# Performance work log

Measured on AMD Instinct MI355X. Metric: run time of the kernel, lower is better.

The kernel has to match this reference:

```python
import jax, jax.numpy as jnp
import numpy as np

# Log-barrier hyperparameters (match torch module defaults / init_kwargs)
K_ITER = 30
MU = 0.01
LR = 1.0
BACKTRACK = 0.5
MAX_LS = 25
EPS = 1e-06

B, S, M, N = 32, 16, 128, 256


def setup_inputs() -> dict:
    key = jax.random.key(0)
    k1, k2, k3 = jax.random.split(key, 3)
    A = jax.random.uniform(k1, (B, S, M, N), dtype=jnp.float32)  # nonnegative rows
    x_star = jax.random.uniform(k2, (B, S, N), dtype=jnp.float32)  # interior point
    b = jnp.einsum('bsmn,bsn->bsm', A, x_star) + 0.5  # strictly feasible polytope
    x_raw = jax.random.normal(k3, (B, S, N), dtype=jnp.float32)
    lower = jnp.zeros((B, S, N), dtype=jnp.float32)
    return {"x_raw": x_raw, "A": A, "b": b, "lower": lower}


def _feasible(x, A_w, b_w, lower):
    # strict feasibility: A x <= b - eps and x >= lower + eps   -> [B,S,1] bool
    Ax = jnp.einsum('bsmn,bsn->bsm', A_w, x)
    c1 = jnp.all(Ax <= b_w - EPS, axis=-1, keepdims=True)
    c2 = jnp.all(x >= lower + EPS, axis=-1, keepdims=True)
    return c1 & c2


def reference(x_raw, A, b, lower):
    # row-normalize constraints (row_normalize=True)
    row_norm = jnp.maximum(jnp.linalg.norm(A, axis=-1, keepdims=True), 1e-12)
    A_w = A / row_norm
    b_w = b / row_norm[..., 0]

    # Deterministic interior-point init (replaces per-sample CPU cvxpy Chebyshev LP):
    # x = lower + t*1 with t = 0.5 * max step along ones-direction staying feasible.
    Ad = jnp.sum(A_w, axis=-1)                                   # [B,S,m] = A_w @ 1
    s = b_w - jnp.einsum('bsmn,bsn->bsm', A_w, lower)            # slack at lower
    ratio = jnp.where(Ad > 0, s / jnp.maximum(Ad, 1e-12), jnp.inf)
    t = 0.5 * jnp.min(ratio, axis=-1, keepdims=True)             # [B,S,1]
    t = jnp.maximum(t, 2.0 * EPS)
    x = lower + t

    # feasibility repair branch (faithful to module; no-op for our inputs)
    feas = _feasible(x, A_w, b_w, lower)
    x = jnp.where(feas, x, 0.5 * (jnp.maximum(x, 0.0) + lower))

    steps = LR * (BACKTRACK ** jnp.arange(MAX_LS, dtype=jnp.float32))  # [L]

    def body(x, _):
        Ax = jnp.einsum('bsmn,bsn->bsm', A_w, x)
        slack = jnp.maximum(b_w - Ax, 1e-12)
        g_bar = jnp.einsum('bsmn,bsm->bsn', A_w, MU / slack)
        s_lo = jnp.maximum(x - lower, 1e-12)
        grad = (x - x_raw) + g_bar + MU / s_lo

        # backtracking line search with GLOBAL ok.all() acceptance (as in torch)
        cand = x[None] - steps[:, None, None, None] * grad[None]       # [L,B,S,n]
        Axc = jnp.einsum('bsmn,lbsn->lbsm', A_w, cand)
        ok = (jnp.all(Axc <= b_w[None] - EPS, axis=-1)
              & jnp.all(cand >= (lower + EPS)[None], axis=-1))          # [L,B,S]
        ok_all = jnp.all(ok, axis=(1, 2))                               # [L]
        found = jnp.any(ok_all)
        idx = jnp.argmax(ok_all)                                        # first accepted step
        w = jax.nn.one_hot(idx, MAX_LS, dtype=x.dtype) * found.astype(x.dtype)
        x_new = jnp.tensordot(w, cand, axes=1) + (1.0 - found.astype(x.dtype)) * x
        return x_new, None

    x, _ = jax.lax.scan(body, x, None, length=K_ITER)
    return jnp.maximum(x, 0.0)
```

## Files before the change

kernel.cpp:

```cpp
#include <hip/hip_runtime.h>

#define K_ITER   30
#define MU       0.01f
#define EPS      1e-6f
#define MAX_LS   25
#define FULLMASK 0x01FFFFFFu
#define MM       128
#define NN       256
#define NPROB    512
#define NTHR     512

#define LSTRIDE 32
#define NBC     16
#define W_FLAG(p)  ((p)*LSTRIDE)
#define W_BCAST(i) (NPROB*LSTRIDE + (i)*LSTRIDE)
#define W_END      (NPROB*LSTRIDE + NBC*LSTRIDE)

#define RED64_AND(v) do { v &= __shfl_xor(v, 1);  v &= __shfl_xor(v, 2);  v &= __shfl_xor(v, 4); \
                          v &= __shfl_xor(v, 8);  v &= __shfl_xor(v, 16); v &= __shfl_xor(v, 32); } while (0)
#define RED64_OR(v)  do { v |= __shfl_xor(v, 1);  v |= __shfl_xor(v, 2);  v |= __shfl_xor(v, 4); \
                          v |= __shfl_xor(v, 8);  v |= __shfl_xor(v, 16); v |= __shfl_xor(v, 32); } while (0)
#define RED64_MIN(v) do { v = fminf(v, __shfl_xor(v, 1));  v = fminf(v, __shfl_xor(v, 2)); \
                          v = fminf(v, __shfl_xor(v, 4));  v = fminf(v, __shfl_xor(v, 8)); \
                          v = fminf(v, __shfl_xor(v, 16)); v = fminf(v, __shfl_xor(v, 32)); } while (0)

#define AGLOAD(p)     __hip_atomic_load((p),      __ATOMIC_RELAXED, __HIP_MEMORY_SCOPE_AGENT)
#define AGSTORE(p, v) __hip_atomic_store((p), (v), __ATOMIC_RELAXED, __HIP_MEMORY_SCOPE_AGENT)

__device__ __forceinline__ float red16_add(float v) {
    v += __int_as_float(__builtin_amdgcn_update_dpp(0, __float_as_int(v), 0x128, 0xF, 0xF, false));
    v += __int_as_float(__builtin_amdgcn_update_dpp(0, __float_as_int(v), 0x124, 0xF, 0xF, false));
    v += __int_as_float(__builtin_amdgcn_update_dpp(0, __float_as_int(v), 0x122, 0xF, 0xF, false));
    v += __int_as_float(__builtin_amdgcn_update_dpp(0, __float_as_int(v), 0x121, 0xF, 0xF, false));
    return v;
}

__global__ void lbp_ws_init(unsigned* __restrict__ wsu)
{
    const int idx = blockIdx.x * 1024 + threadIdx.x;
    if (idx < W_END) wsu[idx] = 0u;
}

__global__ __launch_bounds__(NTHR, 4)
void lbp_fused(const float* __restrict__ xraw_g,
               const float* __restrict__ A_g,
               const float* __restrict__ b_g,
               const float* __restrict__ lower_g,
               float* __restrict__ out_g,
               unsigned* __restrict__ wsu)
{
    const int p    = blockIdx.x;
    const int t    = threadIdx.x;
    const int lane = t & 63;
    const int wave = t >> 6;
    const int g    = lane >> 4;
    const int j    = lane & 15;
    const int wb   = wave * 16;

    const float* A = A_g + (size_t)p * (MM * NN);

    __shared__ __align__(16) float s_x[NN];
    __shared__ __align__(16) float s_grad[NN];
    __shared__ __align__(16) float s_xraw[NN];
    __shared__ __align__(16) float s_lower[NN];
    __shared__ __align__(16) float s_p1g[32][NN];
    __shared__ float s_pg[MM], s_px[MM];
    __shared__ float s_redw[8];
    __shared__ unsigned s_redu[8];
    __shared__ unsigned s_mask, s_gm;
    __shared__ float s_step, s_t0;

    float4 a[4][4];
    {
        const float* base = A + (size_t)(wb + 4 * g) * NN + 4 * j;
        #pragma unroll
        for (int r = 0; r < 4; ++r)
            #pragma unroll
            for (int c = 0; c < 4; ++c)
                a[r][c] = *(const float4*)(base + r * NN + 64 * c);
    }

    if (t < NN) { s_xraw[t] = xraw_g[p * NN + t]; s_lower[t] = lower_g[p * NN + t]; }

    float bbr[4];
    #pragma unroll
    for (int r = 0; r < 4; ++r) bbr[r] = b_g[p * MM + wb + 4 * g + r];

    const float stepj0 = ldexpf(1.0f, -j);

    if (t == 0) { s_mask = 0xFFFFFFFFu; s_step = 0.0f; }
    __syncthreads();

    float cer[4], clr[4];
    {
        float ssq[4] = {0.f,0.f,0.f,0.f}, rs[4] = {0.f,0.f,0.f,0.f}, al[4] = {0.f,0.f,0.f,0.f};
        #pragma unroll
        for (int c = 0; c < 4; ++c) {
            const float4 lo4 = ((const float4*)s_lower)[j + 16 * c];
            #pragma unroll
            for (int r = 0; r < 4; ++r) {
                const float4 av = a[r][c];
                ssq[r] += av.x*av.x + av.y*av.y + av.z*av.z + av.w*av.w;
                rs[r]  += av.x + av.y + av.z + av.w;
                al[r]  += av.x*lo4.x + av.y*lo4.y + av.z*lo4.z + av.w*lo4.w;
            }
        }
        float alr[4], rsr[4];
        float rmin = INFINITY;
        #pragma unroll
        for (int r = 0; r < 4; ++r) {
            const float ssqs = red16_add(ssq[r]);
            const float rss  = red16_add(rs[r]);
            const float als  = red16_add(al[r]);
            const float rr = fmaxf(sqrtf(ssqs), 1e-12f);
            clr[r] = 1e-12f * rr;
            cer[r] = bbr[r] - EPS * rr;
            const float adw = rss / rr;
            const float sw  = (bbr[r] - als) / rr;
            const float ratio = (adw > 0.f) ? (sw / fmaxf(adw, 1e-12f)) : INFINITY;
            rmin = fminf(rmin, ratio);
            alr[r] = als; rsr[r] = rss;
        }
        RED64_MIN(rmin);
        if (lane == 0) s_redw[wave] = rmin;
        __syncthreads();
        if (t == 0) {
            float m = s_redw[0];
            #pragma unroll
            for (int w = 1; w < 8; ++w) m = fminf(m, s_redw[w]);
            s_t0 = fmaxf(0.5f * m, 2.0f * EPS);
        }
        __syncthreads();
        const float t0v = s_t0;
        float xi = 0.f;
        if (t < NN) { xi = s_lower[t] + t0v; s_x[t] = xi; }
        float axc0[4];
        #pragma unroll
        for (int r = 0; r < 4; ++r) {
            axc0[r] = alr[r] + t0v * rsr[r];
            if (j == 0) { s_px[wb + 4 * g + r] = axc0[r]; s_pg[wb + 4 * g + r] = 0.f; }
        }

        int okf = 1;
        #pragma unroll
        for (int r = 0; r < 4; ++r) okf = okf && (axc0[r] <= cer[r]);
        if (t < NN) okf = okf && (xi >= s_lower[t] + EPS);
        const int feas = __syncthreads_and(okf);
        if (!feas) {
            if (t < NN) s_x[t] = 0.5f * (fmaxf(s_x[t], 0.f) + s_lower[t]);
            __syncthreads();
            float axp[4] = {0.f,0.f,0.f,0.f};
            #pragma unroll
            for (int c = 0; c < 4; ++c) {
                const float4 x4 = ((const float4*)s_x)[j + 16 * c];
                #pragma unroll
                for (int r = 0; r < 4; ++r) {
                    const float4 av = a[r][c];
                    axp[r] += av.x*x4.x + av.y*x4.y + av.z*x4.z + av.w*x4.w;
                }
            }
            #pragma unroll
            for (int r = 0; r < 4; ++r) {
                const float s = red16_add(axp[r]);
                if (j == 0) s_px[wb + 4 * g + r] = s;
            }
            __syncthreads();
        }
    }

    for (int k = 0; k < K_ITER; ++k) {
        {
            const float stp = s_step;
            float wm[4];
            #pragma unroll
            for (int r = 0; r < 4; ++r) {
                const int m = wb + 4 * g + r;
                const float axm = s_px[m] - stp * s_pg[m];
                wm[r] = MU / fmaxf(bbr[r] - axm, clr[r]);
            }
            #pragma unroll
            for (int c = 0; c < 4; ++c) {
                float4 gb;
                gb.x = a[0][c].x*wm[0] + a[1][c].x*wm[1] + a[2][c].x*wm[2] + a[3][c].x*wm[3];
                gb.y = a[0][c].y*wm[0] + a[1][c].y*wm[1] + a[2][c].y*wm[2] + a[3][c].y*wm[3];
                gb.z = a[0][c].z*wm[0] + a[1][c].z*wm[1] + a[2][c].z*wm[2] + a[3][c].z*wm[3];
                gb.w = a[0][c].w*wm[0] + a[1][c].w*wm[1] + a[2][c].w*wm[2] + a[3][c].w*wm[3];
                ((float4*)s_p1g[wave * 4 + g])[j + 16 * c] = gb;
            }
        }
        __syncthreads();

        if (t < NN) {
            float gsum = 0.f;
            #pragma unroll
            for (int q = 0; q < 32; ++q) gsum += s_p1g[q][t];
            const float xt = s_x[t];
            const float gr = (xt - s_xraw[t]) + gsum + MU / fmaxf(xt - s_lower[t], 1e-12f);
            s_grad[t] = gr;
            unsigned mn = 0u;
            const float loe = s_lower[t] + EPS;
            float st = 1.0f;
            #pragma unroll
            for (int l = 0; l < MAX_LS; ++l) {
                if (xt - st * gr >= loe) mn |= (1u << l);
                st *= 0.5f;
            }
            RED64_AND(mn);
            if (lane == 0) atomicAnd(&s_mask, mn);
        }
        __syncthreads();

        {
            float pg[4] = {0.f,0.f,0.f,0.f}, px[4] = {0.f,0.f,0.f,0.f};
            #pragma unroll
            for (int c = 0; c < 4; ++c) {
                const float4 g4 = ((const float4*)s_grad)[j + 16 * c];
                const float4 x4 = ((const float4*)s_x)[j + 16 * c];
                #pragma unroll
                for (int r = 0; r < 4; ++r) {
                    const float4 av = a[r][c];
                    pg[r] += av.x*g4.x + av.y*g4.y + av.z*g4.z + av.w*g4.w;
                    px[r] += av.x*x4.x + av.y*x4.y + av.z*x4.z + av.w*x4.w;
                }
            }
            unsigned mand = 0xFFFFFFFFu;
            #pragma unroll
            for (int r = 0; r < 4; ++r) {
                const float pgs = red16_add(pg[r]);
                const float pxs = red16_add(px[r]);
                if (j == 0) { s_pg[wb + 4 * g + r] = pgs; s_px[wb + 4 * g + r] = pxs; }
                const bool ok0 = (pxs - stepj0 * pgs) <= cer[r];
                const bool ok1 = (pxs - (stepj0 * 0x1p-16f) * pgs) <= cer[r];
                const unsigned long long b0 = __ballot(ok0);
                const unsigned long long b1 = __ballot(ok1);
                const unsigned f = ((unsigned)(b0 >> (16 * g)) & 0xFFFFu)
                                 | (((unsigned)(b1 >> (16 * g)) & 0x1FFu) << 16);
                mand &= (f | 0xFE000000u);
            }
            mand &= __shfl_xor(mand, 16);
            mand &= __shfl_xor(mand, 32);
            if (lane == 0) atomicAnd(&s_mask, mand);
        }
        __syncthreads();

        const unsigned tag = (unsigned)(k + 1) << 25;
        if (p == 0) {
            unsigned bad;
            if (t == 0) {
                bad = (~s_mask) & FULLMASK;
            } else {
                unsigned v;
                while ((((v = AGLOAD(&wsu[W_FLAG(t)])) >> 25)) != (unsigned)(k + 1))
                    __builtin_amdgcn_s_sleep(1);
                bad = v & FULLMASK;
            }
            RED64_OR(bad);
            if (lane == 0) s_redu[wave] = bad;
            __syncthreads();
            if (t == 0) {
                unsigned orall = 0u;
                #pragma unroll
                for (int w = 0; w < 8; ++w) orall |= s_redu[w];
                const unsigned gm = FULLMASK & ~orall;
                s_gm   = gm;
                s_step = gm ? ldexpf(1.0f, -(__ffs(gm) - 1)) : 0.0f;
                s_mask = 0xFFFFFFFFu;
            }
            __syncthreads();
            if (t < NBC) AGSTORE(&wsu[W_BCAST(t)], tag | s_gm);
        } else {
            if (t == 0) {
                AGSTORE(&wsu[W_FLAG(p)], tag | ((~s_mask) & FULLMASK));
                s_mask = 0xFFFFFFFFu;
                unsigned v;
                while ((((v = AGLOAD(&wsu[W_BCAST(p & (NBC - 1))])) >> 25)) != (unsigned)(k + 1))
                    __builtin_amdgcn_s_sleep(1);
                const unsigned gm = v & FULLMASK;
                s_step = gm ? ldexpf(1.0f, -(__ffs(gm) - 1)) : 0.0f;
            }
            __syncthreads();
        }

        if (t < NN) s_x[t] -= s_step * s_grad[t];
    }

    if (t < NN) out_g[p * NN + t] = fmaxf(s_x[t], 0.0f);
}

extern "C" void kernel_launch(void* const* d_in, const int* in_sizes, int n_in,
                              void* d_out, int out_size, void* d_ws, size_t ws_size,
                              hipStream_t stream) {
    const float* xraw  = (const float*)d_in[0];
    const float* A     = (const float*)d_in[1];
    const float* b     = (const float*)d_in[2];
    const float* lower = (const float*)d_in[3];
    float* out = (float*)d_out;
    unsigned* wsu = (unsigned*)d_ws;

    lbp_ws_init<<<(W_END + 1023) / 1024, 1024, 0, stream>>>(wsu);
    lbp_fused<<<NPROB, NTHR, 0, stream>>>(xraw, A, b, lower, out, wsu);
}
```

Before: 270.5 us.

## Track Ax incrementally, split gradient column reduction, and shorten the broadcast path

Ax is now kept up to date from the previous Ax minus step times A·grad, so the per-iteration A·x matvec and its reductions are dropped. The 32-partial gradient column sum is split across all 512 threads in halves combined with a shuffle. The coordinator block raises its wave priority and writes the broadcast flags directly from thread 0, removing one barrier. Incremental Ax can drift numerically from the exact product over 30 iterations, which may change feasibility decisions near the boundary.

```diff
diff --git a/kernel.cpp b/kernel.cpp
--- a/kernel.cpp
+++ b/kernel.cpp
@@ -64,10 +64,10 @@
     __shared__ __align__(16) float s_xraw[NN];
     __shared__ __align__(16) float s_lower[NN];
     __shared__ __align__(16) float s_p1g[32][NN];
-    __shared__ float s_pg[MM], s_px[MM];
+    __shared__ float s_ax[MM], s_pg[MM];
     __shared__ float s_redw[8];
     __shared__ unsigned s_redu[8];
-    __shared__ unsigned s_mask, s_gm;
+    __shared__ unsigned s_mask;
     __shared__ float s_step, s_t0;
 
     float4 a[4][4];
@@ -138,7 +138,7 @@
         #pragma unroll
         for (int r = 0; r < 4; ++r) {
             axc0[r] = alr[r] + t0v * rsr[r];
-            if (j == 0) { s_px[wb + 4 * g + r] = axc0[r]; s_pg[wb + 4 * g + r] = 0.f; }
+            if (j == 0) { s_ax[wb + 4 * g + r] = axc0[r]; s_pg[wb + 4 * g + r] = 0.f; }
         }
 
         int okf = 1;
@@ -162,21 +162,26 @@
             #pragma unroll
             for (int r = 0; r < 4; ++r) {
                 const float s = red16_add(axp[r]);
-                if (j == 0) s_px[wb + 4 * g + r] = s;
+                if (j == 0) s_ax[wb + 4 * g + r] = s;
             }
             __syncthreads();
         }
     }
 
     for (int k = 0; k < K_ITER; ++k) {
+        float axm[4];
         {
             const float stp = s_step;
             float wm[4];
             #pragma unroll
             for (int r = 0; r < 4; ++r) {
                 const int m = wb + 4 * g + r;
-                const float axm = s_px[m] - stp * s_pg[m];
-                wm[r] = MU / fmaxf(bbr[r] - axm, clr[r]);
+                axm[r] = s_ax[m] - stp * s_pg[m];
+                wm[r]  = MU / fmaxf(bbr[r] - axm[r], clr[r]);
+            }
+            if (j == 0) {
+                #pragma unroll
+                for (int r = 0; r < 4; ++r) s_ax[wb + 4 * g + r] = axm[r];
             }
             #pragma unroll
             for (int c = 0; c < 4; ++c) {
@@ -190,15 +195,18 @@
         }
         __syncthreads();
 
-        if (t < NN) {
+        {
+            const int col  = t >> 1;
+            const int half = t & 1;
             float gsum = 0.f;
             #pragma unroll
-            for (int q = 0; q < 32; ++q) gsum += s_p1g[q][t];
-            const float xt = s_x[t];
-            const float gr = (xt - s_xraw[t]) + gsum + MU / fmaxf(xt - s_lower[t], 1e-12f);
-            s_grad[t] = gr;
+            for (int q = 0; q < 16; ++q) gsum += s_p1g[half * 16 + q][col];
+            gsum += __shfl_xor(gsum, 1);
+            const float xt = s_x[col];
+            const float gr = (xt - s_xraw[col]) + gsum + MU / fmaxf(xt - s_lower[col], 1e-12f);
+            if (half == 0) s_grad[col] = gr;
             unsigned mn = 0u;
-            const float loe = s_lower[t] + EPS;
+            const float loe = s_lower[col] + EPS;
             float st = 1.0f;
             #pragma unroll
             for (int l = 0; l < MAX_LS; ++l) {
@@ -211,26 +219,23 @@
         __syncthreads();
 
         {
-            float pg[4] = {0.f,0.f,0.f,0.f}, px[4] = {0.f,0.f,0.f,0.f};
+            float pg[4] = {0.f,0.f,0.f,0.f};
             #pragma unroll
             for (int c = 0; c < 4; ++c) {
                 const float4 g4 = ((const float4*)s_grad)[j + 16 * c];
-                const float4 x4 = ((const float4*)s_x)[j + 16 * c];
                 #pragma unroll
                 for (int r = 0; r < 4; ++r) {
                     const float4 av = a[r][c];
                     pg[r] += av.x*g4.x + av.y*g4.y + av.z*g4.z + av.w*g4.w;
-                    px[r] += av.x*x4.x + av.y*x4.y + av.z*x4.z + av.w*x4.w;
                 }
             }
             unsigned mand = 0xFFFFFFFFu;
             #pragma unroll
             for (int r = 0; r < 4; ++r) {
                 const float pgs = red16_add(pg[r]);
-                const float pxs = red16_add(px[r]);
-                if (j == 0) { s_pg[wb + 4 * g + r] = pgs; s_px[wb + 4 * g + r] = pxs; }
-                const bool ok0 = (pxs - stepj0 * pgs) <= cer[r];
-                const bool ok1 = (pxs - (stepj0 * 0x1p-16f) * pgs) <= cer[r];
+                if (j == 0) s_pg[wb + 4 * g + r] = pgs;
+                const bool ok0 = (axm[r] - stepj0 * pgs) <= cer[r];
+                const bool ok1 = (axm[r] - (stepj0 * 0x1p-16f) * pgs) <= cer[r];
                 const unsigned long long b0 = __ballot(ok0);
                 const unsigned long long b1 = __ballot(ok1);
                 const unsigned f = ((unsigned)(b0 >> (16 * g)) & 0xFFFFu)
@@ -245,6 +250,7 @@
 
         const unsigned tag = (unsigned)(k + 1) << 25;
         if (p == 0) {
+            __builtin_amdgcn_s_setprio(1);
             unsigned bad;
             if (t == 0) {
                 bad = (~s_mask) & FULLMASK;
@@ -262,12 +268,14 @@
                 #pragma unroll
                 for (int w = 0; w < 8; ++w) orall |= s_redu[w];
                 const unsigned gm = FULLMASK & ~orall;
-                s_gm   = gm;
+                #pragma unroll
+                for (int i = 0; i < NBC; ++i)
+                    AGSTORE(&wsu[W_BCAST(i)], tag | gm);
                 s_step = gm ? ldexpf(1.0f, -(__ffs(gm) - 1)) : 0.0f;
                 s_mask = 0xFFFFFFFFu;
             }
-            __syncthreads();
-            if (t < NBC) AGSTORE(&wsu[W_BCAST(t)], tag | s_gm);
+            __builtin_amdgcn_s_setprio(0);
+            __syncthreads();
         } else {
             if (t == 0) {
                 AGSTORE(&wsu[W_FLAG(p)], tag | ((~s_mask) & FULLMASK));
```

Result: faster. 242.2 us (median of 2 runs) (-10.5%).
